# Optimization experiments

Hardware: AMD Instinct MI355X
Metric: run time of the kernel (lower is better)

The kernel has to match this reference:

```python
import jax, jax.numpy as jnp
import numpy as np

# init config (from init_kwargs)
NUM_ANCHORS = 5
NUM_CLASSES = 80
ANCHORS = jnp.array([[0.57273, 0.677385], [1.87446, 2.06253], [3.33843, 5.47434],
                     [7.88282, 3.52778], [9.77052, 9.16828]], dtype=jnp.float32)
MAX_BOXES = 50  # hard-coded loop bound in build_targets


def setup_inputs() -> dict:
    key = jax.random.key(0)
    k1, k2 = jax.random.split(key)
    output = jax.random.normal(k1, (64, 425, 38, 38), dtype=jnp.float32)
    # target: (nB, 50*5) of [cls, cx, cy, w, h] normalized to (0,1); strictly
    # positive entries -> all 50 boxes valid (original loop breaks at first 0).
    target = jax.random.uniform(k2, (64, 250), dtype=jnp.float32, minval=0.02, maxval=0.98)
    return {"output": output, "target": target, "reqd_class_index": 14}


def _cls_mask(target, nH, nW):
    """Vectorized build_targets: only cls_mask affects the returned loss.
    For each valid GT box, best anchor = argmax IoU of (0,0,aw,ah) vs (0,0,gw,gh)
    (first max wins, matching the strict > in the Python loop); mark cell
    (b, best_n, gj, gi)."""
    nB = target.shape[0]
    tgt = target.reshape(nB, MAX_BOXES, 5)
    # loop breaks at first t with target[b][5t+1]==0 -> cumulative validity
    valid = jnp.cumprod((tgt[:, :, 1] != 0).astype(jnp.int32), axis=1) > 0
    gx = tgt[:, :, 1] * nW
    gy = tgt[:, :, 2] * nH
    gw = tgt[:, :, 3] * nW  # (nB, T)
    gh = tgt[:, :, 4] * nH
    gi = jnp.clip(jnp.floor(gx).astype(jnp.int32), 0, nW - 1)
    gj = jnp.clip(jnp.floor(gy).astype(jnp.int32), 0, nH - 1)
    aw, ah = ANCHORS[:, 0], ANCHORS[:, 1]  # (nA,)
    # centered-box IoU: intersection widths are min of the widths
    inter = jnp.minimum(gw[..., None], aw) * jnp.minimum(gh[..., None], ah)  # (nB,T,nA)
    iou = inter / (gw[..., None] * gh[..., None] + aw * ah - inter)
    best_n = jnp.argmax(iou, axis=-1).astype(jnp.int32)  # (nB, T), first-max tiebreak
    b = jnp.arange(nB, dtype=jnp.int32)[:, None]
    flat = ((b * NUM_ANCHORS + best_n) * nH + gj) * nW + gi  # (nB, T)
    n_cells = nB * NUM_ANCHORS * nH * nW
    mask = jnp.zeros((n_cells,), jnp.int32).at[flat.ravel()].max(valid.ravel().astype(jnp.int32))
    return mask > 0


def reference(output, target, reqd_class_index):
    nB, _, nH, nW = output.shape
    out = output.reshape(nB, NUM_ANCHORS, 5 + NUM_CLASSES, nH, nW)
    # class logits -> (nB, nA, nH, nW, nC), matching torch's
    # view(nB*nA, nC, nH*nW).transpose(1,2).view(-1, nC) flattening order
    cls_logits = jnp.transpose(out[:, :, 5:, :, :], (0, 1, 3, 4, 2))
    probs = jax.nn.softmax(cls_logits, axis=-1)
    p = probs[..., reqd_class_index].reshape(-1)  # prob of required class per cell
    mask = _cls_mask(target, nH, nW)
    m = mask.astype(p.dtype)
    # L1Loss(cls_prob2, 0, size_average=True) over selected cells == masked mean
    loss = jnp.sum(p * m) / jnp.sum(m)
    max_class_prob = jnp.max(jnp.where(mask, p, -jnp.inf))
    return loss, max_class_prob
```

## Files before the change

### kernel.cpp

```cpp
#include <hip/hip_runtime.h>
#include <stdint.h>
#include <math.h>

#define NUM_ANCHORS 5
#define NUM_CLASSES 80
#define MAX_BOXES   50


__global__ void init_ws(uint32_t* ws, int n_words) {
    int i = threadIdx.x;
    if (i < n_words) ws[i] = (i == 2) ? 0xFF800000u : 0u;
}

__global__ void build_list(const float* __restrict__ target,
                           uint32_t* __restrict__ cnt,
                           int* __restrict__ list,
                           int nH, int nW) {
#pragma clang fp contract(off)
    int b = blockIdx.x;
    int lane = threadIdx.x;
    const float* t = target + (long)b * MAX_BOXES * 5;
    float x = 1.0f, y = 0.0f, w = 0.0f, h = 0.0f;
    if (lane < MAX_BOXES) {
        x = t[lane * 5 + 1];
        y = t[lane * 5 + 2];
        w = t[lane * 5 + 3];
        h = t[lane * 5 + 4];
    }
    unsigned long long zb = __ballot(lane < MAX_BOXES && x == 0.0f);
    int first_zero = zb ? (__ffsll(zb) - 1) : MAX_BOXES;
    bool valid = (lane < MAX_BOXES) && (lane < first_zero);

    int flat = -1 - lane;
    if (valid) {
        float gx = x * (float)nW;
        float gy = y * (float)nH;
        float gw = w * (float)nW;
        float gh = h * (float)nH;
        int gi = min(max((int)floorf(gx), 0), nW - 1);
        int gj = min(max((int)floorf(gy), 0), nH - 1);
        const float aw[NUM_ANCHORS] = {0.57273f, 1.87446f, 3.33843f, 7.88282f, 9.77052f};
        const float ah[NUM_ANCHORS] = {0.677385f, 2.06253f, 5.47434f, 3.52778f, 9.16828f};
        int best = 0; float bestiou = -1.0f;
        #pragma unroll
        for (int n = 0; n < NUM_ANCHORS; ++n) {
            float inter = fminf(gw, aw[n]) * fminf(gh, ah[n]);
            float uni   = gw * gh + aw[n] * ah[n] - inter;
            float iou   = inter / uni;
            if (iou > bestiou) { bestiou = iou; best = n; }
        }
        flat = ((b * NUM_ANCHORS + best) * nH + gj) * nW + gi;
    }
    bool dup = false;
    #pragma unroll
    for (int j = 0; j < MAX_BOXES; ++j) {
        int fj = __shfl(flat, j, 64);
        if (j < lane && fj == flat) dup = true;
    }
    bool keep = valid && !dup;
    unsigned long long kb = __ballot(keep);
    if (keep) {
        int rank = __popcll(kb & ((1ull << lane) - 1ull));
        list[b * MAX_BOXES + rank] = flat;
    }
    if (lane == 0) cnt[b] = (uint32_t)__popcll(kb);
}

__global__ void __launch_bounds__(256)
reduce_fused(const float* __restrict__ output,
             const uint32_t* __restrict__ cnt,
             const int* __restrict__ list,
             float* __restrict__ sumf,
             int* __restrict__ maxbits,
             uint32_t* __restrict__ ticket,
             const int* __restrict__ reqd,
             float* __restrict__ out,
             int HW, int nB) {
    __shared__ float sp[4];
    __shared__ float sm[4];
    int lane = threadIdx.x & 63;
    int wave = threadIdx.x >> 6;
    int g = blockIdx.x * 4 + wave;
    int b = g / MAX_BOXES;
    int i = g - b * MAX_BOXES;
    float p = 0.0f, pm = -INFINITY;
    if (b < nB && i < (int)cnt[b]) {
        int cell = list[g];
        int ba = cell / HW;
        int hw = cell - ba * HW;
        const float* ptr = output + ((long)(ba * (5 + NUM_CLASSES) + 5)) * HW + hw;
        float v0 = ptr[(long)lane * HW];
        float v1 = (lane < NUM_CLASSES - 64) ? ptr[(long)(lane + 64) * HW] : -INFINITY;
        float mx = fmaxf(v0, v1);
        #pragma unroll
        for (int off = 32; off; off >>= 1) mx = fmaxf(mx, __shfl_xor(mx, off, 64));
        float e0 = expf(v0 - mx);
        float e1 = (lane < NUM_CLASSES - 64) ? expf(v1 - mx) : 0.0f;
        float s = e0 + e1;
        #pragma unroll
        for (int off = 32; off; off >>= 1) s += __shfl_xor(s, off, 64);
        int rq = *reqd;
        float lr = (rq < 64) ? __shfl(v0, rq, 64) : __shfl(v1, rq - 64, 64);
        p = expf(lr - mx) / s;
        pm = p;
    }
    if (lane == 0) { sp[wave] = p; sm[wave] = pm; }
    __syncthreads();
    if (threadIdx.x == 0) {
        float ts = 0.0f, tm = -INFINITY;
        #pragma unroll
        for (int w = 0; w < 4; ++w) { ts += sp[w]; tm = fmaxf(tm, sm[w]); }
        if (tm > -INFINITY) {
            atomicAdd(sumf, ts);
            atomicMax(maxbits, __float_as_int(tm));
        }
        __threadfence();
        uint32_t t = atomicAdd(ticket, 1u);
        if (t == (uint32_t)(gridDim.x - 1)) {
            float s  = atomicAdd(sumf, 0.0f);
            int   mb = atomicMax(maxbits, (int)0x80000000);
            int total = 0;
            for (int bb = 0; bb < nB; ++bb) total += (int)cnt[bb];
            out[0] = s / (float)total;
            out[1] = __int_as_float(mb);
        }
    }
}

extern "C" void kernel_launch(void* const* d_in, const int* in_sizes, int n_in,
                              void* d_out, int out_size, void* d_ws, size_t ws_size,
                              hipStream_t stream) {
    const float* output = (const float*)d_in[0];
    const float* target = (const float*)d_in[1];
    const int*   reqd   = (const int*)d_in[2];
    float* out = (float*)d_out;

    int nB = in_sizes[1] / (MAX_BOXES * 5);
    int HW = in_sizes[0] / (nB * (5 + NUM_CLASSES) * NUM_ANCHORS);
    int nW = 1; while (nW * nW < HW) ++nW;
    int nH = HW / nW;

    uint32_t* ws   = (uint32_t*)d_ws;
    float*    sumf = (float*)ws;
    uint32_t* tick = ws + 1;
    int*      maxb = (int*)(ws + 2);
    uint32_t* cnt  = ws + 4;
    int*      list = (int*)(ws + 4 + nB);

    int n_words = 4 + nB;
    init_ws<<<1, 128, 0, stream>>>(ws, n_words);

    build_list<<<nB, 64, 0, stream>>>(target, cnt, list, nH, nW);

    int slots = nB * MAX_BOXES;
    int rblocks = (slots + 3) / 4;
    reduce_fused<<<rblocks, 256, 0, stream>>>(output, cnt, list, sumf, maxb,
                                              tick, reqd, out, HW, nB);
}
```

Baseline: 227.4 us.

## Fuse target-list construction into the softmax reduction kernel

```diff
diff --git a/kernel.cpp b/kernel.cpp
--- a/kernel.cpp
+++ b/kernel.cpp
@@ -7,75 +7,22 @@
 #define MAX_BOXES   50
 
 
-__global__ void init_ws(uint32_t* ws, int n_words) {
+__global__ void init_ws(uint32_t* ws) {
     int i = threadIdx.x;
-    if (i < n_words) ws[i] = (i == 2) ? 0xFF800000u : 0u;
-}
-
-__global__ void build_list(const float* __restrict__ target,
-                           uint32_t* __restrict__ cnt,
-                           int* __restrict__ list,
-                           int nH, int nW) {
-#pragma clang fp contract(off)
-    int b = blockIdx.x;
-    int lane = threadIdx.x;
-    const float* t = target + (long)b * MAX_BOXES * 5;
-    float x = 1.0f, y = 0.0f, w = 0.0f, h = 0.0f;
-    if (lane < MAX_BOXES) {
-        x = t[lane * 5 + 1];
-        y = t[lane * 5 + 2];
-        w = t[lane * 5 + 3];
-        h = t[lane * 5 + 4];
-    }
-    unsigned long long zb = __ballot(lane < MAX_BOXES && x == 0.0f);
-    int first_zero = zb ? (__ffsll(zb) - 1) : MAX_BOXES;
-    bool valid = (lane < MAX_BOXES) && (lane < first_zero);
-
-    int flat = -1 - lane;
-    if (valid) {
-        float gx = x * (float)nW;
-        float gy = y * (float)nH;
-        float gw = w * (float)nW;
-        float gh = h * (float)nH;
-        int gi = min(max((int)floorf(gx), 0), nW - 1);
-        int gj = min(max((int)floorf(gy), 0), nH - 1);
-        const float aw[NUM_ANCHORS] = {0.57273f, 1.87446f, 3.33843f, 7.88282f, 9.77052f};
-        const float ah[NUM_ANCHORS] = {0.677385f, 2.06253f, 5.47434f, 3.52778f, 9.16828f};
-        int best = 0; float bestiou = -1.0f;
-        #pragma unroll
-        for (int n = 0; n < NUM_ANCHORS; ++n) {
-            float inter = fminf(gw, aw[n]) * fminf(gh, ah[n]);
-            float uni   = gw * gh + aw[n] * ah[n] - inter;
-            float iou   = inter / uni;
-            if (iou > bestiou) { bestiou = iou; best = n; }
-        }
-        flat = ((b * NUM_ANCHORS + best) * nH + gj) * nW + gi;
-    }
-    bool dup = false;
-    #pragma unroll
-    for (int j = 0; j < MAX_BOXES; ++j) {
-        int fj = __shfl(flat, j, 64);
-        if (j < lane && fj == flat) dup = true;
-    }
-    bool keep = valid && !dup;
-    unsigned long long kb = __ballot(keep);
-    if (keep) {
-        int rank = __popcll(kb & ((1ull << lane) - 1ull));
-        list[b * MAX_BOXES + rank] = flat;
-    }
-    if (lane == 0) cnt[b] = (uint32_t)__popcll(kb);
+    if (i < 4) ws[i] = (i == 2) ? 0xFF800000u : 0u;
 }
 
 __global__ void __launch_bounds__(256)
-reduce_fused(const float* __restrict__ output,
-             const uint32_t* __restrict__ cnt,
-             const int* __restrict__ list,
-             float* __restrict__ sumf,
-             int* __restrict__ maxbits,
-             uint32_t* __restrict__ ticket,
-             const int* __restrict__ reqd,
-             float* __restrict__ out,
-             int HW, int nB) {
+fused_all(const float* __restrict__ output,
+          const float* __restrict__ target,
+          const int* __restrict__ reqd,
+          float* __restrict__ sumf,
+          int* __restrict__ maxbits,
+          uint32_t* __restrict__ ticket,
+          uint32_t* __restrict__ total,
+          float* __restrict__ out,
+          int HW, int nH, int nW, int nB) {
+#pragma clang fp contract(off)
     __shared__ float sp[4];
     __shared__ float sm[4];
     int lane = threadIdx.x & 63;
@@ -83,26 +30,71 @@
     int g = blockIdx.x * 4 + wave;
     int b = g / MAX_BOXES;
     int i = g - b * MAX_BOXES;
+
     float p = 0.0f, pm = -INFINITY;
-    if (b < nB && i < (int)cnt[b]) {
-        int cell = list[g];
-        int ba = cell / HW;
-        int hw = cell - ba * HW;
-        const float* ptr = output + ((long)(ba * (5 + NUM_CLASSES) + 5)) * HW + hw;
-        float v0 = ptr[(long)lane * HW];
-        float v1 = (lane < NUM_CLASSES - 64) ? ptr[(long)(lane + 64) * HW] : -INFINITY;
-        float mx = fmaxf(v0, v1);
+    if (b < nB) {
+        const float* t = target + (long)b * MAX_BOXES * 5;
+        float x = 1.0f, y = 0.0f, w = 0.0f, h = 0.0f;
+        if (lane < MAX_BOXES) {
+            x = t[lane * 5 + 1];
+            y = t[lane * 5 + 2];
+            w = t[lane * 5 + 3];
+            h = t[lane * 5 + 4];
+        }
+        unsigned long long zb = __ballot(lane < MAX_BOXES && x == 0.0f);
+        int first_zero = zb ? (__ffsll(zb) - 1) : MAX_BOXES;
+        bool valid = (lane < MAX_BOXES) && (lane < first_zero);
+
+        int flat = -1 - lane;
+        if (valid) {
+            float gx = x * (float)nW;
+            float gy = y * (float)nH;
+            float gw = w * (float)nW;
+            float gh = h * (float)nH;
+            int gi = min(max((int)floorf(gx), 0), nW - 1);
+            int gj = min(max((int)floorf(gy), 0), nH - 1);
+            const float aw[NUM_ANCHORS] = {0.57273f, 1.87446f, 3.33843f, 7.88282f, 9.77052f};
+            const float ah[NUM_ANCHORS] = {0.677385f, 2.06253f, 5.47434f, 3.52778f, 9.16828f};
+            int best = 0; float bestiou = -1.0f;
+            #pragma unroll
+            for (int n = 0; n < NUM_ANCHORS; ++n) {
+                float inter = fminf(gw, aw[n]) * fminf(gh, ah[n]);
+                float uni   = gw * gh + aw[n] * ah[n] - inter;
+                float iou   = inter / uni;
+                if (iou > bestiou) { bestiou = iou; best = n; }
+            }
+            flat = ((b * NUM_ANCHORS + best) * nH + gj) * nW + gi;
+        }
+        bool dup = false;
         #pragma unroll
-        for (int off = 32; off; off >>= 1) mx = fmaxf(mx, __shfl_xor(mx, off, 64));
-        float e0 = expf(v0 - mx);
-        float e1 = (lane < NUM_CLASSES - 64) ? expf(v1 - mx) : 0.0f;
-        float s = e0 + e1;
-        #pragma unroll
-        for (int off = 32; off; off >>= 1) s += __shfl_xor(s, off, 64);
-        int rq = *reqd;
-        float lr = (rq < 64) ? __shfl(v0, rq, 64) : __shfl(v1, rq - 64, 64);
-        p = expf(lr - mx) / s;
-        pm = p;
+        for (int j = 0; j < MAX_BOXES; ++j) {
+            int fj = __shfl(flat, j, 64);
+            if (j < lane && fj == flat) dup = true;
+        }
+        unsigned long long kb = __ballot(valid && !dup);
+
+        if (i == 0 && lane == 0) atomicAdd(total, (uint32_t)__popcll(kb));
+
+        if ((kb >> i) & 1ull) {
+            int cell = __shfl(flat, i, 64);
+            int ba = cell / HW;
+            int hw = cell - ba * HW;
+            const float* ptr = output + ((long)(ba * (5 + NUM_CLASSES) + 5)) * HW + hw;
+            float v0 = ptr[(long)lane * HW];
+            float v1 = (lane < NUM_CLASSES - 64) ? ptr[(long)(lane + 64) * HW] : -INFINITY;
+            float mx = fmaxf(v0, v1);
+            #pragma unroll
+            for (int off = 32; off; off >>= 1) mx = fmaxf(mx, __shfl_xor(mx, off, 64));
+            float e0 = expf(v0 - mx);
+            float e1 = (lane < NUM_CLASSES - 64) ? expf(v1 - mx) : 0.0f;
+            float s = e0 + e1;
+            #pragma unroll
+            for (int off = 32; off; off >>= 1) s += __shfl_xor(s, off, 64);
+            int rq = *reqd;
+            float lr = (rq < 64) ? __shfl(v0, rq, 64) : __shfl(v1, rq - 64, 64);
+            p = expf(lr - mx) / s;
+            pm = p;
+        }
     }
     if (lane == 0) { sp[wave] = p; sm[wave] = pm; }
     __syncthreads();
@@ -117,11 +109,10 @@
         __threadfence();
         uint32_t t = atomicAdd(ticket, 1u);
         if (t == (uint32_t)(gridDim.x - 1)) {
-            float s  = atomicAdd(sumf, 0.0f);
-            int   mb = atomicMax(maxbits, (int)0x80000000);
-            int total = 0;
-            for (int bb = 0; bb < nB; ++bb) total += (int)cnt[bb];
-            out[0] = s / (float)total;
+            float    s  = atomicAdd(sumf, 0.0f);
+            int      mb = atomicMax(maxbits, (int)0x80000000);
+            uint32_t tc = atomicAdd(total, 0u);
+            out[0] = s / (float)tc;
             out[1] = __int_as_float(mb);
         }
     }
@@ -144,16 +135,12 @@
     float*    sumf = (float*)ws;
     uint32_t* tick = ws + 1;
     int*      maxb = (int*)(ws + 2);
-    uint32_t* cnt  = ws + 4;
-    int*      list = (int*)(ws + 4 + nB);
+    uint32_t* totl = ws + 3;
 
-    int n_words = 4 + nB;
-    init_ws<<<1, 128, 0, stream>>>(ws, n_words);
-
-    build_list<<<nB, 64, 0, stream>>>(target, cnt, list, nH, nW);
+    init_ws<<<1, 64, 0, stream>>>(ws);
 
     int slots = nB * MAX_BOXES;
     int rblocks = (slots + 3) / 4;
-    reduce_fused<<<rblocks, 256, 0, stream>>>(output, cnt, list, sumf, maxb,
-                                              tick, reqd, out, HW, nB);
+    fused_all<<<rblocks, 256, 0, stream>>>(output, target, reqd, sumf, maxb,
+                                           tick, totl, out, HW, nH, nW, nB);
 }
```

After: 225.3 us. No clear change (-0.9%).
